# Performance work log

Hardware: AMD Instinct MI355X
Metric: run time of the kernel (lower is better)

## Reference

```python
import jax, jax.numpy as jnp
import numpy as np

HEADS = 8


def setup_inputs() -> dict:
    key = jax.random.key(0)
    k1, k2, k3 = jax.random.split(key, 3)
    b, n, d = 4, 2048, 256
    x = jax.random.normal(k1, (b, n, d), dtype=jnp.float32)
    # torch Linear weight is [out, in]; we store transposed [in, out] for x @ W
    w_qkv = jax.random.normal(k2, (d, 3 * d), dtype=jnp.float32) * (d ** -0.5)
    b_qkv = jnp.zeros((3 * d,), dtype=jnp.float32)
    w_out = jax.random.normal(k3, (d, d), dtype=jnp.float32) * (d ** -0.5)
    b_out = jnp.zeros((d,), dtype=jnp.float32)
    return {"x": x, "w_qkv": w_qkv, "b_qkv": b_qkv, "w_out": w_out, "b_out": b_out}


def reference(x, w_qkv, b_qkv, w_out, b_out):
    b, n, d = x.shape
    h = HEADS
    dh = d // h
    scale = d ** -0.5  # NOTE: original scales by full dim**-0.5, not head_dim
    qkv = x @ w_qkv + b_qkv                      # [b, n, 3d]
    q, k, v = jnp.split(qkv, 3, axis=-1)         # each [b, n, d]
    to_heads = lambda t: t.reshape(b, n, h, dh).transpose(0, 2, 1, 3)  # [b,h,n,dh]
    q, k, v = to_heads(q), to_heads(k), to_heads(v)
    dots = jnp.einsum('bhid,bhjd->bhij', q, k) * scale   # [b,h,n,n]
    attn = jax.nn.softmax(dots, axis=-1)
    out = jnp.einsum('bhij,bhjd->bhid', attn, v)         # [b,h,n,dh]
    out = out.transpose(0, 2, 1, 3).reshape(b, n, d)     # [b,n,d]
    return out @ w_out + b_out  # dropout is identity in eval mode
```

## Files before the change

kernel.cpp:

```cpp
#include <hip/hip_runtime.h>
#include <hip/hip_bf16.h>
#include <math.h>

#define BATCH  4
#define SEQ    2048
#define DMODEL 256
#define NH     8
#define DH     32
#define MTOT   (BATCH*SEQ)
#define QSCALE 0.09016844005556021f

typedef short  bf16x8 __attribute__((ext_vector_type(8)));
typedef float  f32x4  __attribute__((ext_vector_type(4)));

static __device__ __forceinline__ ushort f2bf(float f) {
    __hip_bfloat16 h = __float2bfloat16(f);
    return __builtin_bit_cast(ushort, h);
}
static __device__ __forceinline__ uint rne2(float a, float b) {
    uint ua = __builtin_bit_cast(uint, a);
    uint ub = __builtin_bit_cast(uint, b);
    ua += 0x7FFFu + ((ua >> 16) & 1u);
    ub += 0x7FFFu + ((ub >> 16) & 1u);
    return __builtin_amdgcn_perm(ub, ua, 0x07060302);
}
static __device__ __forceinline__ uint pk2(float a, float b) {
#if __has_builtin(__builtin_amdgcn_cvt_pk_bf16_f32)
    auto r = __builtin_amdgcn_cvt_pk_bf16_f32(a, b);
    return __builtin_bit_cast(uint, r);
#else
    return rne2(a, b);
#endif
}

#define LSQ 72
#define KS_STRIDE 40
#define VT_STRIDE 136
#define P_STRIDE  136

__global__ __launch_bounds__(256) void wcvt_all(
    const float* __restrict__ wq, const float* __restrict__ wo,
    const float* __restrict__ x,
    ushort* __restrict__ wqT, ushort* __restrict__ woT,
    ushort* __restrict__ xbf)
{
    const int t  = threadIdx.x;
    const int bx = blockIdx.x;
    if (bx >= 32) {
        const size_t base = ((size_t)(bx - 32) * 8 + blockIdx.y) * 4096 + t * 16;
        float4 f0 = *(const float4*)(x + base);
        float4 f1 = *(const float4*)(x + base + 4);
        float4 f2 = *(const float4*)(x + base + 8);
        float4 f3 = *(const float4*)(x + base + 12);
        uint4 w0, w1;
        w0.x = pk2(f0.x, f0.y); w0.y = pk2(f0.z, f0.w);
        w0.z = pk2(f1.x, f1.y); w0.w = pk2(f1.z, f1.w);
        w1.x = pk2(f2.x, f2.y); w1.y = pk2(f2.z, f2.w);
        w1.z = pk2(f3.x, f3.y); w1.w = pk2(f3.z, f3.w);
        *(uint4*)&xbf[base]     = w0;
        *(uint4*)&xbf[base + 8] = w1;
        return;
    }
    __shared__ float T[32][33];
    const float* w; ushort* wT; int N, n0;
    if (bx < 24) { w = wq; wT = wqT; N = 768; n0 = bx * 32; }
    else         { w = wo; wT = woT; N = 256; n0 = (bx - 24) * 32; }
    const int k0 = blockIdx.y * 32;
    {
        int tr = t >> 3, tc = (t & 7) * 4;
        *(float4*)&T[tr][tc] = *(const float4*)(w + (size_t)(k0 + tr) * N + n0 + tc);
    }
    __syncthreads();
    int nl = t >> 3, kq = (t & 7) * 4;
    ushort4 pk;
    pk.x = f2bf(T[kq + 0][nl]); pk.y = f2bf(T[kq + 1][nl]);
    pk.z = f2bf(T[kq + 2][nl]); pk.w = f2bf(T[kq + 3][nl]);
    *(ushort4*)&wT[(size_t)(n0 + nl) * 256 + k0 + kq] = pk;
}

__global__ __launch_bounds__(256, 3) void qkv_gemm(
    const ushort* __restrict__ xb_, const ushort* __restrict__ wT,
    const float* __restrict__ bias,
    ushort* __restrict__ qo, ushort* __restrict__ ko, ushort* __restrict__ vo)
{
    __shared__ ushort As[64 * LSQ];
    __shared__ ushort Bs[128 * LSQ];
    const int tid  = threadIdx.x;
    const int wid  = tid >> 6;
    const int lane = tid & 63;
    const int lq   = lane & 15;
    const int quad = lane >> 4;
    const int wm   = wid & 1;
    const int wn   = wid >> 1;
    const int m0   = blockIdx.y * 64;
    const int n0   = blockIdx.x * 128;
    const bool isV = (blockIdx.x >= 4);

    const int ar0 = tid >> 3,         ac0 = (tid & 7) * 8;
    const int ar1 = (tid + 256) >> 3;
    const int br0 = tid >> 3,         bc0 = (tid & 7) * 8;
    const int br1 = (tid + 256) >> 3;
    const int br2 = (tid + 512) >> 3;
    const int br3 = (tid + 768) >> 3;

    const ushort* xb = xb_ + (size_t)m0 * 256;
    const ushort* wb = wT  + (size_t)n0 * 256;

    f32x4 acc[8];
#pragma unroll
    for (int i = 0; i < 8; ++i) acc[i] = {0.f, 0.f, 0.f, 0.f};

    uint4 ra0 = *(const uint4*)(xb + (size_t)ar0 * 256 + ac0);
    uint4 ra1 = *(const uint4*)(xb + (size_t)ar1 * 256 + ac0);
    uint4 rb0 = *(const uint4*)(wb + (size_t)br0 * 256 + bc0);
    uint4 rb1 = *(const uint4*)(wb + (size_t)br1 * 256 + bc0);
    uint4 rb2 = *(const uint4*)(wb + (size_t)br2 * 256 + bc0);
    uint4 rb3 = *(const uint4*)(wb + (size_t)br3 * 256 + bc0);

    for (int k0 = 0; k0 < 256; k0 += 64) {
        __syncthreads();
        *(uint4*)&As[ar0 * LSQ + ac0] = ra0;
        *(uint4*)&As[ar1 * LSQ + ac0] = ra1;
        *(uint4*)&Bs[br0 * LSQ + bc0] = rb0;
        *(uint4*)&Bs[br1 * LSQ + bc0] = rb1;
        *(uint4*)&Bs[br2 * LSQ + bc0] = rb2;
        *(uint4*)&Bs[br3 * LSQ + bc0] = rb3;
        __syncthreads();

        const int kn = (k0 + 64) & 255;
        ra0 = *(const uint4*)(xb + (size_t)ar0 * 256 + kn + ac0);
        ra1 = *(const uint4*)(xb + (size_t)ar1 * 256 + kn + ac0);
        rb0 = *(const uint4*)(wb + (size_t)br0 * 256 + kn + bc0);
        rb1 = *(const uint4*)(wb + (size_t)br1 * 256 + kn + bc0);
        rb2 = *(const uint4*)(wb + (size_t)br2 * 256 + kn + bc0);
        rb3 = *(const uint4*)(wb + (size_t)br3 * 256 + kn + bc0);

#pragma unroll
        for (int kh = 0; kh < 2; ++kh) {
            bf16x8 af[2], bfg[4];
#pragma unroll
            for (int mi = 0; mi < 2; ++mi)
                af[mi]  = *(const bf16x8*)&As[(wm * 32 + mi * 16 + lq) * LSQ + kh * 32 + quad * 8];
#pragma unroll
            for (int ni = 0; ni < 4; ++ni)
                bfg[ni] = *(const bf16x8*)&Bs[(wn * 64 + ni * 16 + lq) * LSQ + kh * 32 + quad * 8];
            if (isV) {
#pragma unroll
                for (int mi = 0; mi < 2; ++mi)
#pragma unroll
                    for (int ni = 0; ni < 4; ++ni)
                        acc[mi * 4 + ni] = __builtin_amdgcn_mfma_f32_16x16x32_bf16(
                            af[mi], bfg[ni], acc[mi * 4 + ni], 0, 0, 0);
            } else {
#pragma unroll
                for (int ni = 0; ni < 4; ++ni)
#pragma unroll
                    for (int mi = 0; mi < 2; ++mi)
                        acc[ni * 2 + mi] = __builtin_amdgcn_mfma_f32_16x16x32_bf16(
                            bfg[ni], af[mi], acc[ni * 2 + mi], 0, 0, 0);
            }
        }
    }

    if (!isV) {
#pragma unroll
        for (int ni = 0; ni < 4; ++ni) {
            int nb = n0 + wn * 64 + ni * 16 + quad * 4;
            float4 bs = *(const float4*)(bias + nb);
            int h   = (nb >> 5) & 7;
            int dh0 = nb & 31;
            bool  isQ = (nb < 256);
            float sc  = isQ ? QSCALE : 1.0f;
            ushort* dst = isQ ? qo : ko;
#pragma unroll
            for (int mi = 0; mi < 2; ++mi) {
                int m   = m0 + wm * 32 + mi * 16 + lq;
                int b   = m >> 11, seq = m & 2047;
                f32x4 c = acc[ni * 2 + mi];
                ushort4 pk;
                pk.x = f2bf((c[0] + bs.x) * sc); pk.y = f2bf((c[1] + bs.y) * sc);
                pk.z = f2bf((c[2] + bs.z) * sc); pk.w = f2bf((c[3] + bs.w) * sc);
                *(ushort4*)&dst[(((size_t)b * NH + h) * SEQ + seq) * DH + dh0] = pk;
            }
        }
    } else {
#pragma unroll
        for (int ni = 0; ni < 4; ++ni) {
            int n  = n0 + wn * 64 + ni * 16 + lq;
            int h  = (n >> 5) & 7;
            int dh = n & 31;
            float bsc = bias[n];
#pragma unroll
            for (int mi = 0; mi < 2; ++mi) {
                int mb  = m0 + wm * 32 + mi * 16 + quad * 4;
                int b   = mb >> 11, seq = mb & 2047;
                f32x4 c = acc[mi * 4 + ni];
                ushort4 pk;
                pk.x = f2bf(c[0] + bsc); pk.y = f2bf(c[1] + bsc);
                pk.z = f2bf(c[2] + bsc); pk.w = f2bf(c[3] + bsc);
                *(ushort4*)&vo[(((size_t)b * NH + h) * DH + dh) * SEQ + seq] = pk;
            }
        }
    }
}

__global__ __launch_bounds__(256, 2) void attn_mfma(
    const ushort* __restrict__ qb, const ushort* __restrict__ kb,
    const ushort* __restrict__ vtb, ushort* __restrict__ a_bf)
{
    __shared__ ushort Ks[128 * KS_STRIDE];
    __shared__ ushort VsT[32 * VT_STRIDE];
    __shared__ ushort Pl[4 * 32 * P_STRIDE];

    const int tid  = threadIdx.x;
    const int wid  = tid >> 6;
    const int lane = tid & 63;
    const int lq   = lane & 15;
    const int quad = lane >> 4;
    const int h    = blockIdx.y;
    const int b    = blockIdx.z;
    const int bh   = b * NH + h;
    const int q0   = blockIdx.x * 128 + wid * 32;

    const ushort* qbase = qb + ((size_t)bh * SEQ + q0) * DH;
    const bf16x8 qf0 = *(const bf16x8*)(qbase + (size_t)lq * DH + quad * 8);
    const bf16x8 qf1 = *(const bf16x8*)(qbase + (size_t)(16 + lq) * DH + quad * 8);

    const ushort* kbase  = kb  + (size_t)bh * SEQ * DH;
    const ushort* vtbase = vtb + (size_t)bh * DH * SEQ;
    ushort* Pw = Pl + wid * 32 * P_STRIDE;

    const int f0 = tid, f1 = tid + 256;
    const int kgo0 = (f0 >> 2) * DH + (f0 & 3) * 8;
    const int kgo1 = (f1 >> 2) * DH + (f1 & 3) * 8;
    const int klo0 = (f0 >> 2) * KS_STRIDE + (f0 & 3) * 8;
    const int klo1 = (f1 >> 2) * KS_STRIDE + (f1 & 3) * 8;
    const int vgo0 = (f0 >> 4) * SEQ + (f0 & 15) * 8;
    const int vgo1 = (f1 >> 4) * SEQ + (f1 & 15) * 8;
    const int vlo0 = (f0 >> 4) * VT_STRIDE + (f0 & 15) * 8;
    const int vlo1 = (f1 >> 4) * VT_STRIDE + (f1 & 15) * 8;

    uint4 kr0 = *(const uint4*)(kbase  + kgo0);
    uint4 kr1 = *(const uint4*)(kbase  + kgo1);
    uint4 vr0 = *(const uint4*)(vtbase + vgo0);
    uint4 vr1 = *(const uint4*)(vtbase + vgo1);

    f32x4 o0 = {0.f,0.f,0.f,0.f}, o1 = {0.f,0.f,0.f,0.f};
    f32x4 o2 = {0.f,0.f,0.f,0.f}, o3 = {0.f,0.f,0.f,0.f};
    f32x4 la0 = {0.f,0.f,0.f,0.f}, la1 = {0.f,0.f,0.f,0.f};
    const bf16x8 ones = {0x3F80, 0x3F80, 0x3F80, 0x3F80,
                         0x3F80, 0x3F80, 0x3F80, 0x3F80};

    for (int kt = 0; kt < SEQ; kt += 128) {
        __syncthreads();
        *(uint4*)&Ks[klo0]  = kr0;
        *(uint4*)&Ks[klo1]  = kr1;
        *(uint4*)&VsT[vlo0] = vr0;
        *(uint4*)&VsT[vlo1] = vr1;
        __syncthreads();

        {
            const int ktn = (kt + 128) & (SEQ - 1);
            const ushort* kn = kbase  + (size_t)ktn * DH;
            const ushort* vn = vtbase + ktn;
            kr0 = *(const uint4*)(kn + kgo0);
            kr1 = *(const uint4*)(kn + kgo1);
            vr0 = *(const uint4*)(vn + vgo0);
            vr1 = *(const uint4*)(vn + vgo1);
        }

        f32x4 st0[8], st1[8];
#pragma unroll
        for (int t = 0; t < 8; ++t) {
            bf16x8 kf = *(const bf16x8*)&Ks[(t * 16 + lq) * KS_STRIDE + quad * 8];
            f32x4 z = {0.f, 0.f, 0.f, 0.f};
            st0[t] = __builtin_amdgcn_mfma_f32_16x16x32_bf16(kf, qf0, z, 0, 0, 0);
            st1[t] = __builtin_amdgcn_mfma_f32_16x16x32_bf16(kf, qf1, z, 0, 0, 0);
        }

#pragma unroll
        for (int t = 0; t < 8; ++t) {
            uint2 w2;
            w2.x = pk2(__builtin_amdgcn_exp2f(st0[t][0]),
                       __builtin_amdgcn_exp2f(st0[t][1]));
            w2.y = pk2(__builtin_amdgcn_exp2f(st0[t][2]),
                       __builtin_amdgcn_exp2f(st0[t][3]));
            *(uint2*)&Pw[lq * P_STRIDE + t * 16 + quad * 4] = w2;
        }
#pragma unroll
        for (int t = 0; t < 8; ++t) {
            uint2 w2;
            w2.x = pk2(__builtin_amdgcn_exp2f(st1[t][0]),
                       __builtin_amdgcn_exp2f(st1[t][1]));
            w2.y = pk2(__builtin_amdgcn_exp2f(st1[t][2]),
                       __builtin_amdgcn_exp2f(st1[t][3]));
            *(uint2*)&Pw[(16 + lq) * P_STRIDE + t * 16 + quad * 4] = w2;
        }

#pragma unroll
        for (int s = 0; s < 4; ++s) {
            bf16x8 v0 = *(const bf16x8*)&VsT[lq        * VT_STRIDE + s * 32 + quad * 8];
            bf16x8 v1 = *(const bf16x8*)&VsT[(16 + lq) * VT_STRIDE + s * 32 + quad * 8];
            bf16x8 p0 = *(const bf16x8*)&Pw[lq        * P_STRIDE + s * 32 + quad * 8];
            bf16x8 p1 = *(const bf16x8*)&Pw[(16 + lq) * P_STRIDE + s * 32 + quad * 8];
            o0  = __builtin_amdgcn_mfma_f32_16x16x32_bf16(v0,   p0, o0,  0, 0, 0);
            o1  = __builtin_amdgcn_mfma_f32_16x16x32_bf16(v1,   p0, o1,  0, 0, 0);
            o2  = __builtin_amdgcn_mfma_f32_16x16x32_bf16(v0,   p1, o2,  0, 0, 0);
            o3  = __builtin_amdgcn_mfma_f32_16x16x32_bf16(v1,   p1, o3,  0, 0, 0);
            la0 = __builtin_amdgcn_mfma_f32_16x16x32_bf16(ones, p0, la0, 0, 0, 0);
            la1 = __builtin_amdgcn_mfma_f32_16x16x32_bf16(ones, p1, la1, 0, 0, 0);
        }
    }

    float inv0 = 1.0f / la0[0];
    float inv1 = 1.0f / la1[0];
    ushort* dst0 = a_bf + ((size_t)b * SEQ + q0 + lq) * DMODEL + h * DH;
    ushort* dst1 = dst0 + 16 * DMODEL;
    uint2 w0, w1;
    w0.x = pk2(o0[0] * inv0, o0[1] * inv0);
    w0.y = pk2(o0[2] * inv0, o0[3] * inv0);
    w1.x = pk2(o1[0] * inv0, o1[1] * inv0);
    w1.y = pk2(o1[2] * inv0, o1[3] * inv0);
    *(uint2*)&dst0[quad * 4]      = w0;
    *(uint2*)&dst0[16 + quad * 4] = w1;
    w0.x = pk2(o2[0] * inv1, o2[1] * inv1);
    w0.y = pk2(o2[2] * inv1, o2[3] * inv1);
    w1.x = pk2(o3[0] * inv1, o3[1] * inv1);
    w1.y = pk2(o3[2] * inv1, o3[3] * inv1);
    *(uint2*)&dst1[quad * 4]      = w0;
    *(uint2*)&dst1[16 + quad * 4] = w1;
}

__global__ __launch_bounds__(256) void out_gemm(
    const ushort* __restrict__ a, const ushort* __restrict__ wT,
    const float* __restrict__ bias, float* __restrict__ out)
{
    __shared__ ushort As[64 * LSQ];
    __shared__ ushort Bs[64 * LSQ];
    const int tid  = threadIdx.x;
    const int wid  = tid >> 6;
    const int lane = tid & 63;
    const int lq   = lane & 15;
    const int quad = lane >> 4;
    const int wm   = wid & 1;
    const int wn   = wid >> 1;
    const int m0   = blockIdx.y * 64;
    const int n0   = blockIdx.x * 64;

    const int f0 = tid, f1 = tid + 256;
    const int r0 = f0 >> 3, c0 = (f0 & 7) * 8;
    const int r1 = f1 >> 3, c1 = (f1 & 7) * 8;

    const ushort* ab = a  + (size_t)m0 * 256;
    const ushort* wb = wT + (size_t)n0 * 256;

    f32x4 acc[4];
#pragma unroll
    for (int i = 0; i < 4; ++i) acc[i] = {0.f, 0.f, 0.f, 0.f};

    uint4 ra0 = *(const uint4*)(ab + (size_t)r0 * 256 + c0);
    uint4 ra1 = *(const uint4*)(ab + (size_t)r1 * 256 + c1);
    uint4 rb0 = *(const uint4*)(wb + (size_t)r0 * 256 + c0);
    uint4 rb1 = *(const uint4*)(wb + (size_t)r1 * 256 + c1);

    for (int k0 = 0; k0 < 256; k0 += 64) {
        __syncthreads();
        *(uint4*)&As[r0 * LSQ + c0] = ra0;
        *(uint4*)&As[r1 * LSQ + c1] = ra1;
        *(uint4*)&Bs[r0 * LSQ + c0] = rb0;
        *(uint4*)&Bs[r1 * LSQ + c1] = rb1;
        __syncthreads();

        const int kn = (k0 + 64) & 255;
        ra0 = *(const uint4*)(ab + (size_t)r0 * 256 + kn + c0);
        ra1 = *(const uint4*)(ab + (size_t)r1 * 256 + kn + c1);
        rb0 = *(const uint4*)(wb + (size_t)r0 * 256 + kn + c0);
        rb1 = *(const uint4*)(wb + (size_t)r1 * 256 + kn + c1);

#pragma unroll
        for (int kh = 0; kh < 2; ++kh) {
            bf16x8 af[2], bfg[2];
#pragma unroll
            for (int mi = 0; mi < 2; ++mi)
                af[mi]  = *(const bf16x8*)&As[(wm * 32 + mi * 16 + lq) * LSQ + kh * 32 + quad * 8];
#pragma unroll
            for (int ni = 0; ni < 2; ++ni)
                bfg[ni] = *(const bf16x8*)&Bs[(wn * 32 + ni * 16 + lq) * LSQ + kh * 32 + quad * 8];
#pragma unroll
            for (int ni = 0; ni < 2; ++ni)
#pragma unroll
                for (int mi = 0; mi < 2; ++mi)
                    acc[ni * 2 + mi] = __builtin_amdgcn_mfma_f32_16x16x32_bf16(
                        bfg[ni], af[mi], acc[ni * 2 + mi], 0, 0, 0);
        }
    }

#pragma unroll
    for (int ni = 0; ni < 2; ++ni) {
        int nb = n0 + wn * 32 + ni * 16 + quad * 4;
        float4 bs = *(const float4*)(bias + nb);
#pragma unroll
        for (int mi = 0; mi < 2; ++mi) {
            int m = m0 + wm * 32 + mi * 16 + lq;
            f32x4 c = acc[ni * 2 + mi];
            float4 o;
            o.x = c[0] + bs.x; o.y = c[1] + bs.y;
            o.z = c[2] + bs.z; o.w = c[3] + bs.w;
            *(float4*)&out[(size_t)m * DMODEL + nb] = o;
        }
    }
}

extern "C" void kernel_launch(void* const* d_in, const int* in_sizes, int n_in,
                              void* d_out, int out_size, void* d_ws, size_t ws_size,
                              hipStream_t stream) {
    const float* x     = (const float*)d_in[0];
    const float* w_qkv = (const float*)d_in[1];
    const float* b_qkv = (const float*)d_in[2];
    const float* w_out = (const float*)d_in[3];
    const float* b_out = (const float*)d_in[4];
    float* out = (float*)d_out;

    const size_t TSZ = (size_t)MTOT * DMODEL;
    ushort* q_ws = (ushort*)d_ws;
    ushort* k_ws = q_ws + TSZ;
    ushort* v_ws = k_ws + TSZ;
    ushort* a_bf = v_ws + TSZ;
    ushort* xbf  = a_bf + TSZ;
    ushort* wqT  = xbf + TSZ;
    ushort* woT  = wqT + 768 * 256;

    wcvt_all<<<dim3(96, 8), 256, 0, stream>>>(w_qkv, w_out, x, wqT, woT, xbf);
    qkv_gemm<<<dim3(6, 128), 256, 0, stream>>>(xbf, wqT, b_qkv, q_ws, k_ws, v_ws);
    attn_mfma<<<dim3(SEQ / 128, NH, BATCH), 256, 0, stream>>>(
        q_ws, k_ws, v_ws, a_bf);
    out_gemm<<<dim3(4, 128), 256, 0, stream>>>(a_bf, woT, b_out, out);
}
```

Measured before the change: 120.1 us.

## Split attention over key halves with partial outputs and a combine kernel

The attention kernel now splits the key range into two halves, doubling the grid to 1024 blocks, and writes unnormalized fp32 partial outputs and row sums to workspace. A new combine kernel adds the halves, normalizes and emits bf16. The P buffer is also halved by interleaving score computation and PV accumulation in two passes, and launch bounds rise to 4 blocks per CU, aiming at more occupancy and better CU fill. The cost is an extra launch plus roughly 16MB of extra fp32 traffic for the partials.

New measurement: 122.6 us. +2.1%, slower.

```diff
diff --git a/kernel.cpp b/kernel.cpp
--- a/kernel.cpp
+++ b/kernel.cpp
@@ -36,7 +36,7 @@
 #define LSQ 72
 #define KS_STRIDE 40
 #define VT_STRIDE 136
-#define P_STRIDE  136
+#define P2_STRIDE 72
 
 __global__ __launch_bounds__(256) void wcvt_all(
     const float* __restrict__ wq, const float* __restrict__ wo,
@@ -204,31 +204,35 @@
     }
 }
 
-__global__ __launch_bounds__(256, 2) void attn_mfma(
+__global__ __launch_bounds__(256, 4) void attn_mfma(
     const ushort* __restrict__ qb, const ushort* __restrict__ kb,
-    const ushort* __restrict__ vtb, ushort* __restrict__ a_bf)
+    const ushort* __restrict__ vtb,
+    float* __restrict__ Opart, float* __restrict__ Lpart)
 {
     __shared__ ushort Ks[128 * KS_STRIDE];
     __shared__ ushort VsT[32 * VT_STRIDE];
-    __shared__ ushort Pl[4 * 32 * P_STRIDE];
+    __shared__ ushort Pl[4 * 32 * P2_STRIDE];
 
     const int tid  = threadIdx.x;
     const int wid  = tid >> 6;
     const int lane = tid & 63;
     const int lq   = lane & 15;
     const int quad = lane >> 4;
+    const int qt   = blockIdx.x & 15;
+    const int half = blockIdx.x >> 4;
     const int h    = blockIdx.y;
     const int b    = blockIdx.z;
     const int bh   = b * NH + h;
-    const int q0   = blockIdx.x * 128 + wid * 32;
+    const int q0   = qt * 128 + wid * 32;
+    const int kt0  = half * 1024;
 
     const ushort* qbase = qb + ((size_t)bh * SEQ + q0) * DH;
     const bf16x8 qf0 = *(const bf16x8*)(qbase + (size_t)lq * DH + quad * 8);
     const bf16x8 qf1 = *(const bf16x8*)(qbase + (size_t)(16 + lq) * DH + quad * 8);
 
-    const ushort* kbase  = kb  + (size_t)bh * SEQ * DH;
-    const ushort* vtbase = vtb + (size_t)bh * DH * SEQ;
-    ushort* Pw = Pl + wid * 32 * P_STRIDE;
+    const ushort* kbase  = kb  + (size_t)bh * SEQ * DH + (size_t)kt0 * DH;
+    const ushort* vtbase = vtb + (size_t)bh * DH * SEQ + kt0;
+    ushort* Pw = Pl + wid * 32 * P2_STRIDE;
 
     const int f0 = tid, f1 = tid + 256;
     const int kgo0 = (f0 >> 2) * DH + (f0 & 3) * 8;
@@ -251,7 +255,7 @@
     const bf16x8 ones = {0x3F80, 0x3F80, 0x3F80, 0x3F80,
                          0x3F80, 0x3F80, 0x3F80, 0x3F80};
 
-    for (int kt = 0; kt < SEQ; kt += 128) {
+    for (int it = 0; it < 8; ++it) {
         __syncthreads();
         *(uint4*)&Ks[klo0]  = kr0;
         *(uint4*)&Ks[klo1]  = kr1;
@@ -260,75 +264,87 @@
         __syncthreads();
 
         {
-            const int ktn = (kt + 128) & (SEQ - 1);
-            const ushort* kn = kbase  + (size_t)ktn * DH;
-            const ushort* vn = vtbase + ktn;
+            const int koff = ((it + 1) & 7) * 128;
+            const ushort* kn = kbase  + (size_t)koff * DH;
+            const ushort* vn = vtbase + koff;
             kr0 = *(const uint4*)(kn + kgo0);
             kr1 = *(const uint4*)(kn + kgo1);
             vr0 = *(const uint4*)(vn + vgo0);
             vr1 = *(const uint4*)(vn + vgo1);
         }
 
-        f32x4 st0[8], st1[8];
-#pragma unroll
-        for (int t = 0; t < 8; ++t) {
-            bf16x8 kf = *(const bf16x8*)&Ks[(t * 16 + lq) * KS_STRIDE + quad * 8];
-            f32x4 z = {0.f, 0.f, 0.f, 0.f};
-            st0[t] = __builtin_amdgcn_mfma_f32_16x16x32_bf16(kf, qf0, z, 0, 0, 0);
-            st1[t] = __builtin_amdgcn_mfma_f32_16x16x32_bf16(kf, qf1, z, 0, 0, 0);
-        }
-
-#pragma unroll
-        for (int t = 0; t < 8; ++t) {
-            uint2 w2;
-            w2.x = pk2(__builtin_amdgcn_exp2f(st0[t][0]),
-                       __builtin_amdgcn_exp2f(st0[t][1]));
-            w2.y = pk2(__builtin_amdgcn_exp2f(st0[t][2]),
-                       __builtin_amdgcn_exp2f(st0[t][3]));
-            *(uint2*)&Pw[lq * P_STRIDE + t * 16 + quad * 4] = w2;
-        }
-#pragma unroll
-        for (int t = 0; t < 8; ++t) {
-            uint2 w2;
-            w2.x = pk2(__builtin_amdgcn_exp2f(st1[t][0]),
-                       __builtin_amdgcn_exp2f(st1[t][1]));
-            w2.y = pk2(__builtin_amdgcn_exp2f(st1[t][2]),
-                       __builtin_amdgcn_exp2f(st1[t][3]));
-            *(uint2*)&Pw[(16 + lq) * P_STRIDE + t * 16 + quad * 4] = w2;
-        }
-
-#pragma unroll
-        for (int s = 0; s < 4; ++s) {
-            bf16x8 v0 = *(const bf16x8*)&VsT[lq        * VT_STRIDE + s * 32 + quad * 8];
-            bf16x8 v1 = *(const bf16x8*)&VsT[(16 + lq) * VT_STRIDE + s * 32 + quad * 8];
-            bf16x8 p0 = *(const bf16x8*)&Pw[lq        * P_STRIDE + s * 32 + quad * 8];
-            bf16x8 p1 = *(const bf16x8*)&Pw[(16 + lq) * P_STRIDE + s * 32 + quad * 8];
-            o0  = __builtin_amdgcn_mfma_f32_16x16x32_bf16(v0,   p0, o0,  0, 0, 0);
-            o1  = __builtin_amdgcn_mfma_f32_16x16x32_bf16(v1,   p0, o1,  0, 0, 0);
-            o2  = __builtin_amdgcn_mfma_f32_16x16x32_bf16(v0,   p1, o2,  0, 0, 0);
-            o3  = __builtin_amdgcn_mfma_f32_16x16x32_bf16(v1,   p1, o3,  0, 0, 0);
-            la0 = __builtin_amdgcn_mfma_f32_16x16x32_bf16(ones, p0, la0, 0, 0, 0);
-            la1 = __builtin_amdgcn_mfma_f32_16x16x32_bf16(ones, p1, la1, 0, 0, 0);
-        }
-    }
-
-    float inv0 = 1.0f / la0[0];
-    float inv1 = 1.0f / la1[0];
-    ushort* dst0 = a_bf + ((size_t)b * SEQ + q0 + lq) * DMODEL + h * DH;
-    ushort* dst1 = dst0 + 16 * DMODEL;
-    uint2 w0, w1;
-    w0.x = pk2(o0[0] * inv0, o0[1] * inv0);
-    w0.y = pk2(o0[2] * inv0, o0[3] * inv0);
-    w1.x = pk2(o1[0] * inv0, o1[1] * inv0);
-    w1.y = pk2(o1[2] * inv0, o1[3] * inv0);
-    *(uint2*)&dst0[quad * 4]      = w0;
-    *(uint2*)&dst0[16 + quad * 4] = w1;
-    w0.x = pk2(o2[0] * inv1, o2[1] * inv1);
-    w0.y = pk2(o2[2] * inv1, o2[3] * inv1);
-    w1.x = pk2(o3[0] * inv1, o3[1] * inv1);
-    w1.y = pk2(o3[2] * inv1, o3[3] * inv1);
-    *(uint2*)&dst1[quad * 4]      = w0;
-    *(uint2*)&dst1[16 + quad * 4] = w1;
+#pragma unroll
+        for (int pass = 0; pass < 2; ++pass) {
+#pragma unroll
+            for (int tt = 0; tt < 4; ++tt) {
+                const int t = pass * 4 + tt;
+                bf16x8 kf = *(const bf16x8*)&Ks[(t * 16 + lq) * KS_STRIDE + quad * 8];
+                f32x4 z = {0.f, 0.f, 0.f, 0.f};
+                f32x4 s0 = __builtin_amdgcn_mfma_f32_16x16x32_bf16(kf, qf0, z, 0, 0, 0);
+                f32x4 s1 = __builtin_amdgcn_mfma_f32_16x16x32_bf16(kf, qf1, z, 0, 0, 0);
+                uint2 w2;
+                w2.x = pk2(__builtin_amdgcn_exp2f(s0[0]), __builtin_amdgcn_exp2f(s0[1]));
+                w2.y = pk2(__builtin_amdgcn_exp2f(s0[2]), __builtin_amdgcn_exp2f(s0[3]));
+                *(uint2*)&Pw[lq * P2_STRIDE + tt * 16 + quad * 4] = w2;
+                w2.x = pk2(__builtin_amdgcn_exp2f(s1[0]), __builtin_amdgcn_exp2f(s1[1]));
+                w2.y = pk2(__builtin_amdgcn_exp2f(s1[2]), __builtin_amdgcn_exp2f(s1[3]));
+                *(uint2*)&Pw[(16 + lq) * P2_STRIDE + tt * 16 + quad * 4] = w2;
+            }
+#pragma unroll
+            for (int sc = 0; sc < 2; ++sc) {
+                const int vcol = pass * 64 + sc * 32;
+                bf16x8 v0 = *(const bf16x8*)&VsT[lq        * VT_STRIDE + vcol + quad * 8];
+                bf16x8 v1 = *(const bf16x8*)&VsT[(16 + lq) * VT_STRIDE + vcol + quad * 8];
+                bf16x8 p0 = *(const bf16x8*)&Pw[lq        * P2_STRIDE + sc * 32 + quad * 8];
+                bf16x8 p1 = *(const bf16x8*)&Pw[(16 + lq) * P2_STRIDE + sc * 32 + quad * 8];
+                o0  = __builtin_amdgcn_mfma_f32_16x16x32_bf16(v0,   p0, o0,  0, 0, 0);
+                o1  = __builtin_amdgcn_mfma_f32_16x16x32_bf16(v1,   p0, o1,  0, 0, 0);
+                o2  = __builtin_amdgcn_mfma_f32_16x16x32_bf16(v0,   p1, o2,  0, 0, 0);
+                o3  = __builtin_amdgcn_mfma_f32_16x16x32_bf16(v1,   p1, o3,  0, 0, 0);
+                la0 = __builtin_amdgcn_mfma_f32_16x16x32_bf16(ones, p0, la0, 0, 0, 0);
+                la1 = __builtin_amdgcn_mfma_f32_16x16x32_bf16(ones, p1, la1, 0, 0, 0);
+            }
+        }
+    }
+
+    float* od0 = Opart + (size_t)half * MTOT * DMODEL
+               + ((size_t)b * SEQ + q0 + lq) * DMODEL + h * DH;
+    float* od1 = od0 + 16 * DMODEL;
+    *(float4*)&od0[quad * 4]      = make_float4(o0[0], o0[1], o0[2], o0[3]);
+    *(float4*)&od0[16 + quad * 4] = make_float4(o1[0], o1[1], o1[2], o1[3]);
+    *(float4*)&od1[quad * 4]      = make_float4(o2[0], o2[1], o2[2], o2[3]);
+    *(float4*)&od1[16 + quad * 4] = make_float4(o3[0], o3[1], o3[2], o3[3]);
+    if (quad == 0) {
+        float* ld = Lpart + (size_t)half * (BATCH * NH * SEQ) + (size_t)bh * SEQ;
+        ld[q0 + lq]      = la0[0];
+        ld[q0 + 16 + lq] = la1[0];
+    }
+}
+
+__global__ __launch_bounds__(256) void combine(
+    const float* __restrict__ Opart, const float* __restrict__ Lpart,
+    ushort* __restrict__ a_bf)
+{
+    const size_t idx = ((size_t)blockIdx.x * 256 + threadIdx.x) * 8;
+    const int gs = (int)(idx >> 8);
+    const int d0 = (int)(idx & 255);
+    const int b  = gs >> 11;
+    const int s  = gs & 2047;
+    const int h  = d0 >> 5;
+    const size_t lidx = ((size_t)(b * NH + h)) * SEQ + s;
+    const float l   = Lpart[lidx] + Lpart[(size_t)(BATCH * NH * SEQ) + lidx];
+    const float inv = 1.0f / l;
+    const size_t HOFF = (size_t)MTOT * DMODEL;
+    float4 a0 = *(const float4*)(Opart + idx);
+    float4 a1 = *(const float4*)(Opart + idx + 4);
+    float4 b0 = *(const float4*)(Opart + HOFF + idx);
+    float4 b1 = *(const float4*)(Opart + HOFF + idx + 4);
+    uint4 w;
+    w.x = pk2((a0.x + b0.x) * inv, (a0.y + b0.y) * inv);
+    w.y = pk2((a0.z + b0.z) * inv, (a0.w + b0.w) * inv);
+    w.z = pk2((a1.x + b1.x) * inv, (a1.y + b1.y) * inv);
+    w.w = pk2((a1.z + b1.z) * inv, (a1.w + b1.w) * inv);
+    *(uint4*)&a_bf[idx] = w;
 }
 
 __global__ __launch_bounds__(256) void out_gemm(
@@ -429,10 +445,13 @@
     ushort* xbf  = a_bf + TSZ;
     ushort* wqT  = xbf + TSZ;
     ushort* woT  = wqT + 768 * 256;
+    float*  Opart = (float*)(woT + 256 * 256);
+    float*  Lpart = Opart + 2 * TSZ;
 
     wcvt_all<<<dim3(96, 8), 256, 0, stream>>>(w_qkv, w_out, x, wqT, woT, xbf);
     qkv_gemm<<<dim3(6, 128), 256, 0, stream>>>(xbf, wqT, b_qkv, q_ws, k_ws, v_ws);
-    attn_mfma<<<dim3(SEQ / 128, NH, BATCH), 256, 0, stream>>>(
-        q_ws, k_ws, v_ws, a_bf);
+    attn_mfma<<<dim3(32, NH, BATCH), 256, 0, stream>>>(
+        q_ws, k_ws, v_ws, Opart, Lpart);
+    combine<<<dim3(1024), 256, 0, stream>>>(Opart, Lpart, a_bf);
     out_gemm<<<dim3(4, 128), 256, 0, stream>>>(a_bf, woT, b_out, out);
 }
```

## Shrink attention query tile to 16 rows per wave and raise occupancy

Applied to the files above, without the earlier changes.

Each wave in the attention kernel now handles 16 query rows instead of 32, and the grid doubles to 32 blocks per head. The 128-key tile is processed in two 64-key passes, so the P scratch buffer in shared memory shrinks and fewer score registers are live, and launch bounds ask for 4 blocks per CU. The aim is higher occupancy and better latency hiding. In exchange, K and V tiles are loaded twice as often per query, since each block now covers only 64 queries.

Measured after the change: 124.0 us. 3.2% more time.

```diff
diff --git a/kernel.cpp b/kernel.cpp
--- a/kernel.cpp
+++ b/kernel.cpp
@@ -36,7 +36,7 @@
 #define LSQ 72
 #define KS_STRIDE 40
 #define VT_STRIDE 136
-#define P_STRIDE  136
+#define P2_STRIDE 72
 
 __global__ __launch_bounds__(256) void wcvt_all(
     const float* __restrict__ wq, const float* __restrict__ wo,
@@ -204,13 +204,13 @@
     }
 }
 
-__global__ __launch_bounds__(256, 2) void attn_mfma(
+__global__ __launch_bounds__(256, 4) void attn_mfma(
     const ushort* __restrict__ qb, const ushort* __restrict__ kb,
     const ushort* __restrict__ vtb, ushort* __restrict__ a_bf)
 {
     __shared__ ushort Ks[128 * KS_STRIDE];
     __shared__ ushort VsT[32 * VT_STRIDE];
-    __shared__ ushort Pl[4 * 32 * P_STRIDE];
+    __shared__ ushort Pl[4 * 16 * P2_STRIDE];
 
     const int tid  = threadIdx.x;
     const int wid  = tid >> 6;
@@ -220,15 +220,13 @@
     const int h    = blockIdx.y;
     const int b    = blockIdx.z;
     const int bh   = b * NH + h;
-    const int q0   = blockIdx.x * 128 + wid * 32;
-
-    const ushort* qbase = qb + ((size_t)bh * SEQ + q0) * DH;
-    const bf16x8 qf0 = *(const bf16x8*)(qbase + (size_t)lq * DH + quad * 8);
-    const bf16x8 qf1 = *(const bf16x8*)(qbase + (size_t)(16 + lq) * DH + quad * 8);
+    const int q0   = blockIdx.x * 64 + wid * 16;
+
+    const bf16x8 qf = *(const bf16x8*)(qb + ((size_t)bh * SEQ + q0 + lq) * DH + quad * 8);
 
     const ushort* kbase  = kb  + (size_t)bh * SEQ * DH;
     const ushort* vtbase = vtb + (size_t)bh * DH * SEQ;
-    ushort* Pw = Pl + wid * 32 * P_STRIDE;
+    ushort* Pw = Pl + wid * 16 * P2_STRIDE;
 
     const int f0 = tid, f1 = tid + 256;
     const int kgo0 = (f0 >> 2) * DH + (f0 & 3) * 8;
@@ -245,9 +243,9 @@
     uint4 vr0 = *(const uint4*)(vtbase + vgo0);
     uint4 vr1 = *(const uint4*)(vtbase + vgo1);
 
-    f32x4 o0 = {0.f,0.f,0.f,0.f}, o1 = {0.f,0.f,0.f,0.f};
-    f32x4 o2 = {0.f,0.f,0.f,0.f}, o3 = {0.f,0.f,0.f,0.f};
-    f32x4 la0 = {0.f,0.f,0.f,0.f}, la1 = {0.f,0.f,0.f,0.f};
+    f32x4 o0  = {0.f,0.f,0.f,0.f};
+    f32x4 o1  = {0.f,0.f,0.f,0.f};
+    f32x4 la0 = {0.f,0.f,0.f,0.f};
     const bf16x8 ones = {0x3F80, 0x3F80, 0x3F80, 0x3F80,
                          0x3F80, 0x3F80, 0x3F80, 0x3F80};
 
@@ -269,66 +267,41 @@
             vr1 = *(const uint4*)(vn + vgo1);
         }
 
-        f32x4 st0[8], st1[8];
-#pragma unroll
-        for (int t = 0; t < 8; ++t) {
-            bf16x8 kf = *(const bf16x8*)&Ks[(t * 16 + lq) * KS_STRIDE + quad * 8];
-            f32x4 z = {0.f, 0.f, 0.f, 0.f};
-            st0[t] = __builtin_amdgcn_mfma_f32_16x16x32_bf16(kf, qf0, z, 0, 0, 0);
-            st1[t] = __builtin_amdgcn_mfma_f32_16x16x32_bf16(kf, qf1, z, 0, 0, 0);
-        }
-
-#pragma unroll
-        for (int t = 0; t < 8; ++t) {
-            uint2 w2;
-            w2.x = pk2(__builtin_amdgcn_exp2f(st0[t][0]),
-                       __builtin_amdgcn_exp2f(st0[t][1]));
-            w2.y = pk2(__builtin_amdgcn_exp2f(st0[t][2]),
-                       __builtin_amdgcn_exp2f(st0[t][3]));
-            *(uint2*)&Pw[lq * P_STRIDE + t * 16 + quad * 4] = w2;
-        }
-#pragma unroll
-        for (int t = 0; t < 8; ++t) {
-            uint2 w2;
-            w2.x = pk2(__builtin_amdgcn_exp2f(st1[t][0]),
-                       __builtin_amdgcn_exp2f(st1[t][1]));
-            w2.y = pk2(__builtin_amdgcn_exp2f(st1[t][2]),
-                       __builtin_amdgcn_exp2f(st1[t][3]));
-            *(uint2*)&Pw[(16 + lq) * P_STRIDE + t * 16 + quad * 4] = w2;
-        }
-
-#pragma unroll
-        for (int s = 0; s < 4; ++s) {
-            bf16x8 v0 = *(const bf16x8*)&VsT[lq        * VT_STRIDE + s * 32 + quad * 8];
-            bf16x8 v1 = *(const bf16x8*)&VsT[(16 + lq) * VT_STRIDE + s * 32 + quad * 8];
-            bf16x8 p0 = *(const bf16x8*)&Pw[lq        * P_STRIDE + s * 32 + quad * 8];
-            bf16x8 p1 = *(const bf16x8*)&Pw[(16 + lq) * P_STRIDE + s * 32 + quad * 8];
-            o0  = __builtin_amdgcn_mfma_f32_16x16x32_bf16(v0,   p0, o0,  0, 0, 0);
-            o1  = __builtin_amdgcn_mfma_f32_16x16x32_bf16(v1,   p0, o1,  0, 0, 0);
-            o2  = __builtin_amdgcn_mfma_f32_16x16x32_bf16(v0,   p1, o2,  0, 0, 0);
-            o3  = __builtin_amdgcn_mfma_f32_16x16x32_bf16(v1,   p1, o3,  0, 0, 0);
-            la0 = __builtin_amdgcn_mfma_f32_16x16x32_bf16(ones, p0, la0, 0, 0, 0);
-            la1 = __builtin_amdgcn_mfma_f32_16x16x32_bf16(ones, p1, la1, 0, 0, 0);
-        }
-    }
-
-    float inv0 = 1.0f / la0[0];
-    float inv1 = 1.0f / la1[0];
-    ushort* dst0 = a_bf + ((size_t)b * SEQ + q0 + lq) * DMODEL + h * DH;
-    ushort* dst1 = dst0 + 16 * DMODEL;
+#pragma unroll
+        for (int pass = 0; pass < 2; ++pass) {
+#pragma unroll
+            for (int tt = 0; tt < 4; ++tt) {
+                const int t = pass * 4 + tt;
+                bf16x8 kf = *(const bf16x8*)&Ks[(t * 16 + lq) * KS_STRIDE + quad * 8];
+                f32x4 z = {0.f, 0.f, 0.f, 0.f};
+                f32x4 s0 = __builtin_amdgcn_mfma_f32_16x16x32_bf16(kf, qf, z, 0, 0, 0);
+                uint2 w2;
+                w2.x = pk2(__builtin_amdgcn_exp2f(s0[0]), __builtin_amdgcn_exp2f(s0[1]));
+                w2.y = pk2(__builtin_amdgcn_exp2f(s0[2]), __builtin_amdgcn_exp2f(s0[3]));
+                *(uint2*)&Pw[lq * P2_STRIDE + tt * 16 + quad * 4] = w2;
+            }
+#pragma unroll
+            for (int sc = 0; sc < 2; ++sc) {
+                const int vcol = pass * 64 + sc * 32;
+                bf16x8 v0 = *(const bf16x8*)&VsT[lq        * VT_STRIDE + vcol + quad * 8];
+                bf16x8 v1 = *(const bf16x8*)&VsT[(16 + lq) * VT_STRIDE + vcol + quad * 8];
+                bf16x8 p0 = *(const bf16x8*)&Pw[lq * P2_STRIDE + sc * 32 + quad * 8];
+                o0  = __builtin_amdgcn_mfma_f32_16x16x32_bf16(v0,   p0, o0,  0, 0, 0);
+                o1  = __builtin_amdgcn_mfma_f32_16x16x32_bf16(v1,   p0, o1,  0, 0, 0);
+                la0 = __builtin_amdgcn_mfma_f32_16x16x32_bf16(ones, p0, la0, 0, 0, 0);
+            }
+        }
+    }
+
+    float inv = 1.0f / la0[0];
+    ushort* dst = a_bf + ((size_t)b * SEQ + q0 + lq) * DMODEL + h * DH;
     uint2 w0, w1;
-    w0.x = pk2(o0[0] * inv0, o0[1] * inv0);
-    w0.y = pk2(o0[2] * inv0, o0[3] * inv0);
-    w1.x = pk2(o1[0] * inv0, o1[1] * inv0);
-    w1.y = pk2(o1[2] * inv0, o1[3] * inv0);
-    *(uint2*)&dst0[quad * 4]      = w0;
-    *(uint2*)&dst0[16 + quad * 4] = w1;
-    w0.x = pk2(o2[0] * inv1, o2[1] * inv1);
-    w0.y = pk2(o2[2] * inv1, o2[3] * inv1);
-    w1.x = pk2(o3[0] * inv1, o3[1] * inv1);
-    w1.y = pk2(o3[2] * inv1, o3[3] * inv1);
-    *(uint2*)&dst1[quad * 4]      = w0;
-    *(uint2*)&dst1[16 + quad * 4] = w1;
+    w0.x = pk2(o0[0] * inv, o0[1] * inv);
+    w0.y = pk2(o0[2] * inv, o0[3] * inv);
+    w1.x = pk2(o1[0] * inv, o1[1] * inv);
+    w1.y = pk2(o1[2] * inv, o1[3] * inv);
+    *(uint2*)&dst[quad * 4]      = w0;
+    *(uint2*)&dst[16 + quad * 4] = w1;
 }
 
 __global__ __launch_bounds__(256) void out_gemm(
@@ -432,7 +405,7 @@
 
     wcvt_all<<<dim3(96, 8), 256, 0, stream>>>(w_qkv, w_out, x, wqT, woT, xbf);
     qkv_gemm<<<dim3(6, 128), 256, 0, stream>>>(xbf, wqT, b_qkv, q_ws, k_ws, v_ws);
-    attn_mfma<<<dim3(SEQ / 128, NH, BATCH), 256, 0, stream>>>(
+    attn_mfma<<<dim3(32, NH, BATCH), 256, 0, stream>>>(
         q_ws, k_ws, v_ws, a_bf);
     out_gemm<<<dim3(4, 128), 256, 0, stream>>>(a_bf, woT, b_out, out);
 }
```
